# Optimization experiments

Measured on AMD Instinct MI355X. Metric: run time of the kernel, lower is better.

## Reference

```python
import jax, jax.numpy as jnp
import numpy as np

N, E, IN, H, OUT = 100000, 1600000, 64, 64, 10
NEG_SLOPE = 0.2  # PyG GATConv default negative_slope


def _glorot(key, shape):
    fan = sum(shape) if len(shape) > 1 else shape[0]
    return jax.random.normal(key, shape, dtype=jnp.float32) * jnp.sqrt(2.0 / fan)


def setup_inputs() -> dict:
    key = jax.random.key(0)
    ks = jax.random.split(key, 16)
    x = jax.random.normal(ks[0], (N, IN), dtype=jnp.float32)
    edge_index = jax.random.randint(ks[1], (2, E), 0, N, dtype=jnp.int32)
    dims = [(IN, H), (H, H), (H, OUT)]
    params = {}
    for i, (fi, fo) in enumerate(dims, start=1):
        params[f"W{i}"] = _glorot(ks[4 * i - 2], (fi, fo))
        params[f"a{i}s"] = _glorot(ks[4 * i - 1], (fo,))
        params[f"a{i}d"] = _glorot(ks[4 * i], (fo,))
        params[f"b{i}"] = jnp.zeros((fo,), dtype=jnp.float32)
    return {"x": x, "edge_index": edge_index, **params}


def gat_conv(x, src, dst, W, a_s, a_d, b):
    """Single-head GATConv (PyG defaults): gather -> leaky_relu scores ->
    segment softmax over dst -> scatter-add aggregate."""
    n = x.shape[0]
    h = x @ W                                   # [N, Fo]
    alpha_src = h @ a_s                          # [N]
    alpha_dst = h @ a_d                          # [N]
    e = jax.nn.leaky_relu(alpha_src[src] + alpha_dst[dst], NEG_SLOPE)  # [E']
    m = jax.ops.segment_max(e, dst, num_segments=n)                    # stable softmax max
    ex = jnp.exp(e - m[dst])
    denom = jax.ops.segment_sum(ex, dst, num_segments=n)
    alpha = ex / denom[dst]                      # [E'] per-dst softmax
    out = jax.ops.segment_sum(alpha[:, None] * h[src], dst, num_segments=n)
    return out + b


def reference(x, edge_index, W1, a1s, a1d, b1, W2, a2s, a2d, b2, W3, a3s, a3d, b3):
    n = x.shape[0]
    loops = jnp.arange(n, dtype=edge_index.dtype)  # add_self_loops=True
    src = jnp.concatenate([edge_index[0], loops])
    dst = jnp.concatenate([edge_index[1], loops])
    h = jax.nn.relu(gat_conv(x, src, dst, W1, a1s, a1d, b1))
    # dropout is identity at inference (training=False)
    h = jax.nn.relu(gat_conv(h, src, dst, W2, a2s, a2d, b2))
    h = gat_conv(h, src, dst, W3, a3s, a3d, b3)
    return jax.nn.log_softmax(h, axis=1)
```

## Files before the change

### kernel.cpp

```cpp
#include <hip/hip_runtime.h>
#include <math.h>
#include <type_traits>


#define NEG_SLOPE 0.2f
#define BKT_BITS 9
#define BKT_SZ   512
#define PACK_SRC_BITS 20

typedef _Float16 h8v __attribute__((ext_vector_type(8)));
typedef _Float16 h4v __attribute__((ext_vector_type(4)));

__global__ void k_zero(int* p, int n) {
    int i = blockIdx.x * blockDim.x + threadIdx.x;
    if (i < n) p[i] = 0;
}

__global__ __launch_bounds__(256) void k_hist(const int* __restrict__ dst, int E,
                                              int nb, int* __restrict__ bcount) {
    __shared__ int h[BKT_SZ];
    for (int i = threadIdx.x; i < nb; i += 256) h[i] = 0;
    __syncthreads();
    for (int i = blockIdx.x * 256 + threadIdx.x; i < E; i += gridDim.x * 256)
        atomicAdd(&h[dst[i] >> BKT_BITS], 1);
    __syncthreads();
    for (int i = threadIdx.x; i < nb; i += 256)
        if (h[i]) atomicAdd(&bcount[i], h[i]);
}

__global__ __launch_bounds__(512) void k_bscan(const int* __restrict__ bcount, int nb,
                                               int E, int N, int* __restrict__ ebase,
                                               int* __restrict__ gcur,
                                               int* __restrict__ rowptr) {
    __shared__ int sm[BKT_SZ];
    int t = threadIdx.x;
    int v = (t < nb) ? bcount[t] : 0;
    sm[t] = v;
    __syncthreads();
    for (int o = 1; o < BKT_SZ; o <<= 1) {
        int tv = (t >= o) ? sm[t - o] : 0;
        __syncthreads();
        sm[t] += tv;
        __syncthreads();
    }
    int excl = sm[t] - v;
    if (t < nb) {
        ebase[t] = excl;
        gcur[t] = excl;
    }
    if (t == nb - 1) ebase[nb] = excl + v;
    if (t == 0) rowptr[N] = E + N;
}

__global__ __launch_bounds__(1024) void k_bscatter(const int* __restrict__ src,
                                                   const int* __restrict__ dst, int E,
                                                   int nb, int* __restrict__ gcur,
                                                   int* __restrict__ ebuf) {
    __shared__ int lc[BKT_SZ];
    __shared__ int gb[BKT_SZ];
    for (int i = threadIdx.x; i < nb; i += 1024) lc[i] = 0;
    __syncthreads();
    int base = blockIdx.x * 8192;
    int bkt[8], rnk[8], pk[8];
#pragma unroll
    for (int j = 0; j < 8; j++) {
        int i = base + j * 1024 + threadIdx.x;
        bkt[j] = -1;
        if (i < E) {
            int d = dst[i];
            int s = src[i];
            int b = d >> BKT_BITS;
            bkt[j] = b;
            rnk[j] = atomicAdd(&lc[b], 1);
            pk[j] = ((d & (BKT_SZ - 1)) << PACK_SRC_BITS) | s;
        }
    }
    __syncthreads();
    for (int b = threadIdx.x; b < nb; b += 1024)
        if (lc[b]) gb[b] = atomicAdd(&gcur[b], lc[b]);
    __syncthreads();
#pragma unroll
    for (int j = 0; j < 8; j++)
        if (bkt[j] >= 0) ebuf[gb[bkt[j]] + rnk[j]] = pk[j];
}

__global__ __launch_bounds__(512) void k_bcsr(const int* __restrict__ ebuf,
                                              const int* __restrict__ ebase, int N,
                                              int* __restrict__ rowptr,
                                              int* __restrict__ csr) {
    __shared__ int cnt[BKT_SZ];
    __shared__ int sm[BKT_SZ];
    int b = blockIdx.x;
    int t = threadIdx.x;
    int n0 = b << BKT_BITS;
    int nn = min(BKT_SZ, N - n0);
    cnt[t] = 0;
    __syncthreads();
    int e0 = ebase[b], e1 = ebase[b + 1];
    for (int i = e0 + t; i < e1; i += BKT_SZ)
        atomicAdd(&cnt[ebuf[i] >> PACK_SRC_BITS], 1);
    __syncthreads();
    int v = cnt[t] + (t < nn ? 1 : 0);
    sm[t] = v;
    __syncthreads();
    for (int o = 1; o < BKT_SZ; o <<= 1) {
        int tv = (t >= o) ? sm[t - o] : 0;
        __syncthreads();
        sm[t] += tv;
        __syncthreads();
    }
    int excl = sm[t] - v;
    int cb = e0 + n0;
    if (t < nn) {
        rowptr[n0 + t] = cb + excl;
        csr[cb + excl] = n0 + t;
    }
    cnt[t] = excl + 1;
    __syncthreads();
    for (int i = e0 + t; i < e1; i += BKT_SZ) {
        int p = ebuf[i];
        int dl = p >> PACK_SRC_BITS;
        int pos = atomicAdd(&cnt[dl], 1);
        csr[cb + pos] = p & ((1 << PACK_SRC_BITS) - 1);
    }
}

template <int FP>
__global__ __launch_bounds__(256) void k_gemm(
    const float* __restrict__ X, const float* __restrict__ W,
    const float* __restrict__ a_s, const float* __restrict__ a_d,
    int N, int Freal,
    _Float16* __restrict__ H, float* __restrict__ asb, float* __restrict__ adb) {
    int lane = threadIdx.x & 63;
    int lf = lane & (FP - 1);

    float w[64];
#pragma unroll
    for (int k = 0; k < 64; k++)
        w[k] = (lf < Freal) ? W[k * Freal + lf] : 0.f;
    float av = (lf < Freal) ? a_s[lf] : 0.f;
    float dv = (lf < Freal) ? a_d[lf] : 0.f;

    int wid = (blockIdx.x * blockDim.x + threadIdx.x) >> 6;
    int nw = (gridDim.x * blockDim.x) >> 6;

    for (int row = wid; row < N; row += nw) {
        const float* __restrict__ xr =
            X + (size_t)__builtin_amdgcn_readfirstlane(row) * 64;
        float acc = 0.f;
#pragma unroll
        for (int k = 0; k < 64; k++) acc = fmaf(xr[k], w[k], acc);
        if (lane < FP) H[(size_t)row * FP + lane] = (_Float16)acc;
        float ps = (lane < FP) ? acc * av : 0.f;
        float pd = (lane < FP) ? acc * dv : 0.f;
        for (int o = 32; o > 0; o >>= 1) {
            ps += __shfl_xor(ps, o, 64);
            pd += __shfl_xor(pd, o, 64);
        }
        if (lane == 0) {
            asb[row] = ps;
            adb[row] = pd;
        }
    }
}

template <int FP>
__device__ __forceinline__ void agg_slow(
    int node, const _Float16* __restrict__ H, const float* __restrict__ asb,
    const float* __restrict__ adb, const float* __restrict__ bias,
    const int* __restrict__ rowptr, const int* __restrict__ csr,
    int N, int Freal, float* __restrict__ out, int mode, int lane) {
    if (node >= N) return;
    int start = rowptr[node];
    int end = rowptr[node + 1];
    float ad = adb[node];
    int lf = lane & (FP - 1);
    const float NEG_INF = -__builtin_inff();

    float m = NEG_INF;
    for (int base = start; base < end; base += 64) {
        int i = base + lane;
        if (i < end) {
            float t = asb[csr[i]] + ad;
            float e = (t > 0.f) ? t : NEG_SLOPE * t;
            m = fmaxf(m, e);
        }
    }
    for (int o = 32; o > 0; o >>= 1) m = fmaxf(m, __shfl_xor(m, o, 64));
    float dsum = 0.f, acc = 0.f;
    for (int base = start; base < end; base += 64) {
        int i = base + lane;
        int cnt = min(64, end - base);
        int s = 0;
        float p = 0.f;
        if (i < end) {
            s = csr[i];
            float t = asb[s] + ad;
            float e = (t > 0.f) ? t : NEG_SLOPE * t;
            p = __expf(e - m);
        }
        dsum += p;
        for (int j = 0; j < cnt; j++) {
            float pj = __shfl(p, j, 64);
            int sj = __shfl(s, j, 64);
            acc = fmaf(pj, (float)H[(size_t)sj * FP + lf], acc);
        }
    }
    for (int o = 32; o > 0; o >>= 1) dsum += __shfl_xor(dsum, o, 64);

    float b = (lf < Freal) ? bias[lf] : 0.f;
    float z = acc / dsum + b;
    if (mode == 0) {
        if (lane < FP) out[(size_t)node * FP + lane] = fmaxf(z, 0.f);
    } else {
        float zz = (lane < Freal) ? z : NEG_INF;
        float zm = zz;
        for (int o = 32; o > 0; o >>= 1) zm = fmaxf(zm, __shfl_xor(zm, o, 64));
        float ez = (lane < Freal) ? __expf(zz - zm) : 0.f;
        float es = ez;
        for (int o = 32; o > 0; o >>= 1) es += __shfl_xor(es, o, 64);
        if (lane < Freal) out[(size_t)node * Freal + lane] = zz - zm - __logf(es);
    }
}

template <int FP, int W>
__global__ __launch_bounds__(256) void k_agg(
    const _Float16* __restrict__ H, const float* __restrict__ asb,
    const float* __restrict__ adb, const float* __restrict__ bias,
    const int* __restrict__ rowptr, const int* __restrict__ csr,
    int N, int Freal, float* __restrict__ out, int mode) {
    constexpr int LPR = FP / W;
    constexpr int GRPH = 32 / LPR;
    using vecW = typename std::conditional<W == 8, h8v, h4v>::type;
    int lane = threadIdx.x & 63;
    int half = lane >> 5;
    int li = lane & 31;
    int wid = (blockIdx.x * blockDim.x + threadIdx.x) >> 6;
    int nA = 2 * wid;
    if (nA >= N) return;
    int n = nA + half;
    bool valid = (n < N);
    int start = 0, end = 0;
    float ad = 0.f;
    if (valid) {
        start = rowptr[n];
        end = rowptr[n + 1];
        ad = adb[n];
    }
    int deg = end - start;
    int degm = max(deg, __shfl_xor(deg, 32, 64));

    const float NEG_INF = -__builtin_inff();

    if (degm <= 32) {
        int g = li / LPR;
        int fl = li % LPR;
        int s = 0;
        float e = NEG_INF;
        if (li < deg) {
            s = csr[start + li];
            float t = asb[s] + ad;
            e = (t > 0.f) ? t : NEG_SLOPE * t;
        }
        float m = e;
        for (int o = 16; o > 0; o >>= 1) m = fmaxf(m, __shfl_xor(m, o, 64));
        float p = (li < deg) ? __expf(e - m) : 0.f;
        float dsum = p;
        for (int o = 16; o > 0; o >>= 1) dsum += __shfl_xor(dsum, o, 64);

        float acc[W];
#pragma unroll
        for (int c = 0; c < W; c++) acc[c] = 0.f;
#pragma unroll 2
        for (int jb = 0; jb < degm; jb += GRPH) {
            int gidx = half * 32 + jb + g;
            float pj = __shfl(p, gidx, 64);
            int sj = __shfl(s, gidx, 64);
            vecW r = ((const vecW*)(H + (size_t)sj * FP))[fl];
#pragma unroll
            for (int c = 0; c < W; c++) acc[c] = fmaf(pj, (float)r[c], acc[c]);
        }
        for (int o = LPR; o < 32; o <<= 1) {
#pragma unroll
            for (int c = 0; c < W; c++) acc[c] += __shfl_xor(acc[c], o, 64);
        }
        float inv = 1.f / dsum;
        int fbase = fl * W;

        if (mode == 0) {
            if (valid && li < LPR) {
                float z[W];
#pragma unroll
                for (int c = 0; c < W; c++)
                    z[c] = fmaxf(fmaf(acc[c], inv, bias[fbase + c]), 0.f);
                float4* op = (float4*)(out + (size_t)n * FP + fbase);
#pragma unroll
                for (int q = 0; q < W / 4; q++)
                    op[q] = make_float4(z[4 * q], z[4 * q + 1], z[4 * q + 2],
                                        z[4 * q + 3]);
            }
        } else {
            float zc[W];
#pragma unroll
            for (int c = 0; c < W; c++) {
                int f = fbase + c;
                zc[c] = (f < Freal) ? fmaf(acc[c], inv, bias[f]) : NEG_INF;
            }
            float vm = zc[0];
#pragma unroll
            for (int c = 1; c < W; c++) vm = fmaxf(vm, zc[c]);
            for (int o = 1; o < LPR; o <<= 1) vm = fmaxf(vm, __shfl_xor(vm, o, 64));
            float es = 0.f;
#pragma unroll
            for (int c = 0; c < W; c++) es += __expf(zc[c] - vm);
            for (int o = 1; o < LPR; o <<= 1) es += __shfl_xor(es, o, 64);
            float ls = __logf(es);
            if (valid && li < LPR) {
#pragma unroll
                for (int c = 0; c < W; c++) {
                    int f = fbase + c;
                    if (f < Freal) out[(size_t)n * Freal + f] = zc[c] - vm - ls;
                }
            }
        }
    } else {
        agg_slow<FP>(nA, H, asb, adb, bias, rowptr, csr, N, Freal, out, mode, lane);
        agg_slow<FP>(nA + 1, H, asb, adb, bias, rowptr, csr, N, Freal, out, mode, lane);
    }
}

extern "C" void kernel_launch(void* const* d_in, const int* in_sizes, int n_in,
                              void* d_out, int out_size, void* d_ws, size_t ws_size,
                              hipStream_t stream) {
    const float* x = (const float*)d_in[0];
    const int* ei = (const int*)d_in[1];
    const float* W1 = (const float*)d_in[2];
    const float* a1s = (const float*)d_in[3];
    const float* a1d = (const float*)d_in[4];
    const float* b1 = (const float*)d_in[5];
    const float* W2 = (const float*)d_in[6];
    const float* a2s = (const float*)d_in[7];
    const float* a2d = (const float*)d_in[8];
    const float* b2 = (const float*)d_in[9];
    const float* W3 = (const float*)d_in[10];
    const float* a3s = (const float*)d_in[11];
    const float* a3d = (const float*)d_in[12];
    const float* b3 = (const float*)d_in[13];

    const int N = in_sizes[0] / 64;
    const int E = in_sizes[1] / 2;
    const int Etot = E + N;
    const int nb = (N + BKT_SZ - 1) >> BKT_BITS;
    const int* srcv = ei;
    const int* dstv = ei + E;

    size_t off = 0;
    char* base = (char*)d_ws;
    auto carve = [&](size_t bytes) -> void* {
        void* p = base + off;
        off = (off + bytes + 255) & ~(size_t)255;
        return p;
    };
    int* bcount = (int*)carve((size_t)(nb + 1) * 4);
    int* ebase = (int*)carve((size_t)(nb + 1) * 4);
    int* gcur = (int*)carve((size_t)nb * 4);
    int* rowptr = (int*)carve((size_t)(N + 1) * 4);
    int* csr = (int*)carve((size_t)Etot * 4);
    float* asb = (float*)carve((size_t)N * 4);
    float* adb = (float*)carve((size_t)N * 4);
    _Float16* hA = (_Float16*)carve((size_t)N * 64 * 2);
    float* fB = (float*)carve((size_t)N * 64 * 4);
    _Float16* hC = (_Float16*)carve((size_t)N * 16 * 2);
    int* ebuf = (int*)hA;

    k_zero<<<(nb + 255) / 256, 256, 0, stream>>>(bcount, nb);
    k_hist<<<512, 256, 0, stream>>>(dstv, E, nb, bcount);
    k_bscan<<<1, BKT_SZ, 0, stream>>>(bcount, nb, E, N, ebase, gcur, rowptr);
    k_bscatter<<<(E + 8191) / 8192, 1024, 0, stream>>>(srcv, dstv, E, nb, gcur, ebuf);
    k_bcsr<<<nb, BKT_SZ, 0, stream>>>(ebuf, ebase, N, rowptr, csr);

    const int aggBlocks = (N + 7) / 8;
    const int gemmBlocks = 4096;

    k_gemm<64><<<gemmBlocks, 256, 0, stream>>>(x, W1, a1s, a1d, N, 64, hA, asb, adb);
    k_agg<64, 8><<<aggBlocks, 256, 0, stream>>>(hA, asb, adb, b1, rowptr, csr, N, 64, fB, 0);
    k_gemm<64><<<gemmBlocks, 256, 0, stream>>>(fB, W2, a2s, a2d, N, 64, hA, asb, adb);
    k_agg<64, 8><<<aggBlocks, 256, 0, stream>>>(hA, asb, adb, b2, rowptr, csr, N, 64, fB, 0);
    k_gemm<16><<<gemmBlocks, 256, 0, stream>>>(fB, W3, a3s, a3d, N, 10, hC, asb, adb);
    k_agg<16, 4><<<aggBlocks, 256, 0, stream>>>(hC, asb, adb, b3, rowptr, csr, N, 10,
                                                (float*)d_out, 1);
}
```

Measured before the change: 391.7 us.

## Compute node feature GEMM with fp16 MFMA tiles instead of scalar FMAs

Rewrites the per-layer dense projection to process 16-row tiles with the 16x16x32 fp16 MFMA instruction. Weights and inputs are converted to half precision, and the attention-score dot products are computed from the accumulator fragments with a 16-lane shuffle reduction. The old kernel had each wavefront do one row with 64 scalar FMAs per lane. The grid is shrunk to match the tile count. Converting inputs to fp16 lowers GEMM precision, and the GEMM is a small part of the pipeline next to aggregation and CSR build.

After: 341.3 us. 1.15x faster.

```diff
diff --git a/kernel.cpp b/kernel.cpp
--- a/kernel.cpp
+++ b/kernel.cpp
@@ -10,6 +10,7 @@
 
 typedef _Float16 h8v __attribute__((ext_vector_type(8)));
 typedef _Float16 h4v __attribute__((ext_vector_type(4)));
+typedef float f4v __attribute__((ext_vector_type(4)));
 
 __global__ void k_zero(int* p, int n) {
     int i = blockIdx.x * blockDim.x + threadIdx.x;
@@ -131,35 +132,92 @@
     const float* __restrict__ a_s, const float* __restrict__ a_d,
     int N, int Freal,
     _Float16* __restrict__ H, float* __restrict__ asb, float* __restrict__ adb) {
+    constexpr int NT = FP / 16;
     int lane = threadIdx.x & 63;
-    int lf = lane & (FP - 1);
-
-    float w[64];
-#pragma unroll
-    for (int k = 0; k < 64; k++)
-        w[k] = (lf < Freal) ? W[k * Freal + lf] : 0.f;
-    float av = (lf < Freal) ? a_s[lf] : 0.f;
-    float dv = (lf < Freal) ? a_d[lf] : 0.f;
+    int quad = lane >> 4;
+    int c16 = lane & 15;
+
+    h8v bf[NT][2];
+    float asv[NT], adv[NT];
+#pragma unroll
+    for (int nt = 0; nt < NT; nt++) {
+        int n = nt * 16 + c16;
+        bool ok = (n < Freal);
+        asv[nt] = ok ? a_s[n] : 0.f;
+        adv[nt] = ok ? a_d[n] : 0.f;
+#pragma unroll
+        for (int kt = 0; kt < 2; kt++)
+#pragma unroll
+            for (int j = 0; j < 8; j++) {
+                int k = kt * 32 + quad * 8 + j;
+                bf[nt][kt][j] = (_Float16)(ok ? W[k * Freal + n] : 0.f);
+            }
+    }
 
     int wid = (blockIdx.x * blockDim.x + threadIdx.x) >> 6;
     int nw = (gridDim.x * blockDim.x) >> 6;
-
-    for (int row = wid; row < N; row += nw) {
-        const float* __restrict__ xr =
-            X + (size_t)__builtin_amdgcn_readfirstlane(row) * 64;
-        float acc = 0.f;
-#pragma unroll
-        for (int k = 0; k < 64; k++) acc = fmaf(xr[k], w[k], acc);
-        if (lane < FP) H[(size_t)row * FP + lane] = (_Float16)acc;
-        float ps = (lane < FP) ? acc * av : 0.f;
-        float pd = (lane < FP) ? acc * dv : 0.f;
-        for (int o = 32; o > 0; o >>= 1) {
-            ps += __shfl_xor(ps, o, 64);
-            pd += __shfl_xor(pd, o, 64);
-        }
-        if (lane == 0) {
-            asb[row] = ps;
-            adb[row] = pd;
+    int ntile = (N + 15) >> 4;
+
+    for (int t = wid; t < ntile; t += nw) {
+        int m0 = t << 4;
+        int row = m0 + c16;
+        const float* xr = X + (size_t)min(row, N - 1) * 64;
+        h8v af[2];
+#pragma unroll
+        for (int kt = 0; kt < 2; kt++) {
+            f4v x0 = *(const f4v*)(xr + kt * 32 + quad * 8);
+            f4v x1 = *(const f4v*)(xr + kt * 32 + quad * 8 + 4);
+#pragma unroll
+            for (int j = 0; j < 4; j++) {
+                af[kt][j] = (_Float16)x0[j];
+                af[kt][4 + j] = (_Float16)x1[j];
+            }
+        }
+        f4v c[NT];
+#pragma unroll
+        for (int nt = 0; nt < NT; nt++) c[nt] = (f4v){0.f, 0.f, 0.f, 0.f};
+#pragma unroll
+        for (int kt = 0; kt < 2; kt++)
+#pragma unroll
+            for (int nt = 0; nt < NT; nt++)
+                c[nt] = __builtin_amdgcn_mfma_f32_16x16x32_f16(af[kt], bf[nt][kt],
+                                                               c[nt], 0, 0, 0);
+#pragma unroll
+        for (int reg = 0; reg < 4; reg++) {
+            int r = m0 + quad * 4 + reg;
+            if (r < N) {
+#pragma unroll
+                for (int nt = 0; nt < NT; nt++)
+                    H[(size_t)r * FP + nt * 16 + c16] = (_Float16)c[nt][reg];
+            }
+        }
+        float ps[4], pd[4];
+#pragma unroll
+        for (int reg = 0; reg < 4; reg++) {
+            ps[reg] = 0.f;
+            pd[reg] = 0.f;
+#pragma unroll
+            for (int nt = 0; nt < NT; nt++) {
+                ps[reg] = fmaf(c[nt][reg], asv[nt], ps[reg]);
+                pd[reg] = fmaf(c[nt][reg], adv[nt], pd[reg]);
+            }
+        }
+        for (int o = 1; o < 16; o <<= 1) {
+#pragma unroll
+            for (int reg = 0; reg < 4; reg++) {
+                ps[reg] += __shfl_xor(ps[reg], o, 64);
+                pd[reg] += __shfl_xor(pd[reg], o, 64);
+            }
+        }
+        if (c16 == 0) {
+#pragma unroll
+            for (int reg = 0; reg < 4; reg++) {
+                int r = m0 + quad * 4 + reg;
+                if (r < N) {
+                    asb[r] = ps[reg];
+                    adb[r] = pd[reg];
+                }
+            }
         }
     }
 }
@@ -380,7 +438,7 @@
     k_bcsr<<<nb, BKT_SZ, 0, stream>>>(ebuf, ebase, N, rowptr, csr);
 
     const int aggBlocks = (N + 7) / 8;
-    const int gemmBlocks = 4096;
+    const int gemmBlocks = 784;
 
     k_gemm<64><<<gemmBlocks, 256, 0, stream>>>(x, W1, a1s, a1d, N, 64, hA, asb, adb);
     k_agg<64, 8><<<aggBlocks, 256, 0, stream>>>(hA, asb, adb, b1, rowptr, csr, N, 64, fB, 0);
```
